# Kernel optimization log

Hardware: AMD Instinct MI355X
Metric: run time of the kernel (lower is better)

Reference implementation:

```python
import jax, jax.numpy as jnp
import numpy as np

N, E = 20000, 320000
H1, C1 = 8, 128   # gat1 heads/out
H2, C2 = 1, 128   # gat2 heads/out
D_IN = 768
NEG_SLOPE = 0.2
BN_EPS = 1e-5


def setup_inputs() -> dict:
    key = jax.random.key(0)
    ks = jax.random.split(key, 16)
    def rn(k, shape, fan):
        return jax.random.normal(k, shape, dtype=jnp.float32) / np.sqrt(fan)
    x = jax.random.normal(ks[0], (N, D_IN), dtype=jnp.float32)
    edge_index = jax.random.randint(ks[1], (2, E), 0, N, dtype=jnp.int64)
    return {
        "x": x,
        "edge_index": edge_index,
        "W1": rn(ks[2], (D_IN, H1 * C1), D_IN),
        "att_src1": rn(ks[3], (H1, C1), C1),
        "att_dst1": rn(ks[4], (H1, C1), C1),
        "b1": jnp.zeros((H1 * C1,), jnp.float32),
        "W2": rn(ks[5], (H1 * C1, H2 * C2), H1 * C1),
        "att_src2": rn(ks[6], (H2, C2), C2),
        "att_dst2": rn(ks[7], (H2, C2), C2),
        "b2": jnp.zeros((C2,), jnp.float32),
        "g1": jnp.ones((H1 * C1,), jnp.float32),
        "be1": jnp.zeros((H1 * C1,), jnp.float32),
        "g2": jnp.ones((C2,), jnp.float32),
        "be2": jnp.zeros((C2,), jnp.float32),
        "Wc1": rn(ks[8], (C2, 64), C2),
        "bc1": jnp.zeros((64,), jnp.float32),
        "Wc2": rn(ks[9], (64, 2), 64),
        "bc2": jnp.zeros((2,), jnp.float32),
    }


def gat_conv(x, src, dst, W, att_src, att_dst, bias, heads, ch, concat):
    n = x.shape[0]
    h = (x @ W).reshape(n, heads, ch)                      # [N,H,C]
    a_s = jnp.sum(h * att_src[None], axis=-1)              # [N,H]
    a_d = jnp.sum(h * att_dst[None], axis=-1)
    e = a_s[src] + a_d[dst]                                # [Et,H]
    e = jax.nn.leaky_relu(e, NEG_SLOPE)
    # segment softmax over incoming edges of each dst node
    m = jax.ops.segment_max(e, dst, num_segments=n)
    ex = jnp.exp(e - m[dst])
    z = jax.ops.segment_sum(ex, dst, num_segments=n)
    alpha = ex / z[dst]                                    # [Et,H]
    msg = alpha[:, :, None] * h[src]                       # [Et,H,C]
    out = jax.ops.segment_sum(msg, dst, num_segments=n)    # [N,H,C]
    if concat:
        out = out.reshape(n, heads * ch)
    else:
        out = out.mean(axis=1)
    return out + bias


def batch_norm(x, gamma, beta):
    mu = x.mean(axis=0)
    var = x.var(axis=0)
    return (x - mu) * jax.lax.rsqrt(var + BN_EPS) * gamma + beta


def reference(x, edge_index, W1, att_src1, att_dst1, b1, W2, att_src2, att_dst2, b2,
              g1, be1, g2, be2, Wc1, bc1, Wc2, bc2):
    n = x.shape[0]
    loop = jnp.arange(n, dtype=edge_index.dtype)
    src = jnp.concatenate([edge_index[0], loop])  # PyG add_self_loops default
    dst = jnp.concatenate([edge_index[1], loop])
    h = gat_conv(x, src, dst, W1, att_src1, att_dst1, b1, H1, C1, True)
    h = jax.nn.elu(batch_norm(h, g1, be1))
    h = gat_conv(h, src, dst, W2, att_src2, att_dst2, b2, H2, C2, False)
    h = jax.nn.elu(batch_norm(h, g2, be2))
    h = jax.nn.relu(h @ Wc1 + bc1)
    return h @ Wc2 + bc2
```

## Files before the change

### kernel.cpp

```cpp
#include <hip/hip_runtime.h>
#include <hip/hip_bf16.h>
#include <math.h>

#define N_NODES 20000
#define N_EDGES 320000
#define DIN 768
#define F1 1024
#define H1 8
#define C1 128
#define F2 128
#define NEG_SLOPE 0.2f
#define BN_EPS 1e-5f
#define RESCALE_THR 8.0f

typedef __attribute__((ext_vector_type(8))) __bf16 bf16x8;
typedef __attribute__((ext_vector_type(4))) float f32x4;

__device__ __forceinline__ float leaky(float x) { return x > 0.f ? x : NEG_SLOPE * x; }

__device__ __forceinline__ unsigned short f2bu(float x) {
  __hip_bfloat16 b = __float2bfloat16(x);
  return *(unsigned short*)&b;
}
__device__ __forceinline__ float b2f(unsigned short u) {
  return __uint_as_float(((unsigned)u) << 16);
}
__device__ __forceinline__ unsigned pack2(float lo, float hi) {
  return (unsigned)f2bu(lo) | ((unsigned)f2bu(hi) << 16);
}

__device__ __forceinline__ void async_copy16(void* lds, const void* g) {
  __builtin_amdgcn_global_load_lds(
      (const __attribute__((address_space(1))) unsigned int*)g,
      (__attribute__((address_space(3))) unsigned int*)lds, 16, 0, 0);
}

__global__ void repack_hist_kernel(const int* raw, int* ei32, int* deg) {
  int is64 = (raw[1] == 0 && raw[3] == 0 && raw[5] == 0 && raw[7] == 0) ? 1 : 0;
  int e = blockIdx.x * blockDim.x + threadIdx.x;
  if (e < 2 * N_EDGES) {
    int v = is64 ? raw[2 * e] : raw[e];
    ei32[e] = v;
    if (e >= N_EDGES) atomicAdd(&deg[v], 1);
  }
}

#define NPT 20
__global__ __launch_bounds__(1024) void scan_kernel(const int* __restrict__ deg,
                                                    int* __restrict__ off,
                                                    int* __restrict__ cursor) {
  __shared__ int wsum[16];
  int tid = threadIdx.x;
  int lane = tid & 63, wv = tid >> 6;
  int base = tid * NPT;
  int loc[NPT];
  int run = 0;
#pragma unroll
  for (int k = 0; k < NPT; ++k) {
    int i = base + k;
    int v = (i < N_NODES) ? deg[i] : 0;
    loc[k] = run;
    run += v;
  }
  int incl = run;
  for (int sh = 1; sh < 64; sh <<= 1) {
    int t = __shfl_up(incl, sh, 64);
    if (lane >= sh) incl += t;
  }
  if (lane == 63) wsum[wv] = incl;
  __syncthreads();
  if (wv == 0 && lane < 16) {
    int v = wsum[lane];
    for (int sh = 1; sh < 16; sh <<= 1) {
      int t = __shfl_up(v, sh, 16);
      if (lane >= sh) v += t;
    }
    wsum[lane] = v;
  }
  __syncthreads();
  int wbase = (wv > 0) ? wsum[wv - 1] : 0;
  int tbase = wbase + incl - run;
#pragma unroll
  for (int k = 0; k < NPT; ++k) {
    int i = base + k;
    if (i < N_NODES) {
      int o = tbase + loc[k];
      off[i] = o;
      cursor[i] = o;
    }
  }
  if (tid == 1023) off[N_NODES] = wbase + incl;
}

__global__ void scatter_kernel(const int* ei, int* cursor, int* elist) {
  int e = blockIdx.x * blockDim.x + threadIdx.x;
  if (e < N_EDGES) {
    int dst = ei[N_EDGES + e];
    int p = atomicAdd(&cursor[dst], 1);
    elist[p] = ei[e];
  }
}

__global__ void f2b_kernel(const float* __restrict__ in, unsigned short* __restrict__ out,
                           size_t n4) {
  size_t i = (size_t)blockIdx.x * blockDim.x + threadIdx.x;
  size_t stride = (size_t)gridDim.x * blockDim.x;
  for (; i < n4; i += stride) {
    float4 v = ((const float4*)in)[i];
    ushort4 u;
    u.x = f2bu(v.x); u.y = f2bu(v.y); u.z = f2bu(v.z); u.w = f2bu(v.w);
    ((ushort4*)out)[i] = u;
  }
}

__global__ void transpose_b_kernel(const float* __restrict__ W, unsigned short* __restrict__ WT,
                                   int K, int N) {
  __shared__ float t[32][33];
  int k0 = blockIdx.y * 32, n0 = blockIdx.x * 32;
  int tx = threadIdx.x & 31, ty = threadIdx.x >> 5;
  for (int i = 0; i < 32; i += 8)
    t[ty + i][tx] = W[(size_t)(k0 + ty + i) * N + n0 + tx];
  __syncthreads();
  for (int i = 0; i < 32; i += 8)
    WT[(size_t)(n0 + ty + i) * K + k0 + tx] = f2bu(t[tx][ty + i]);
}

#define GBM 128
#define GBN 128
#define GBK 64
template <int H, int SWZ>
__global__ __launch_bounds__(256) void mfma_gemm_att_kernel(
    const unsigned short* __restrict__ A,
    const unsigned short* __restrict__ BT,
    unsigned short* __restrict__ C,
    const float* __restrict__ att_src,
    const float* __restrict__ att_dst,
    float* __restrict__ as_out,
    float* __restrict__ ad_out,
    int M, int N, int K) {
  __shared__ __hip_bfloat16 As[GBM][GBK];
  __shared__ __hip_bfloat16 Bs[GBN][GBK];
  __shared__ float sred[128][2];
  __shared__ float dred[128][2];
  int bx, by;
  if (SWZ) {
    int bid = blockIdx.x;
    int pl = bid & 7, c = (bid >> 3) & 7, ph = bid >> 6;
    int p = ph * 8 + pl;
    if (p * GBM >= M) return;
    by = p; bx = c;
  } else {
    bx = blockIdx.x; by = blockIdx.y;
  }
  int tid = threadIdx.x;
  int lane = tid & 63, wid = tid >> 6;
  int wr = wid >> 1, wc = wid & 1;
  int row0 = by * GBM, col0 = bx * GBN;
  int head = bx;
  int l16 = lane & 15, l4 = lane >> 4;
  f32x4 acc[4][4] = {};
  for (int k0 = 0; k0 < K; k0 += GBK) {
#pragma unroll
    for (int j = 0; j < 4; ++j) {
      int c = j * 256 + tid;
      int r = c >> 3, kk = (c & 7) << 3;
      int ga = row0 + r; if (ga >= M) ga = M - 1;
      async_copy16(&As[r][kk], A + (size_t)ga * K + k0 + kk);
      async_copy16(&Bs[r][kk], BT + (size_t)(col0 + r) * K + k0 + kk);
    }
    __syncthreads();
#pragma unroll
    for (int ks = 0; ks < 2; ++ks) {
      bf16x8 af[4], bfr[4];
#pragma unroll
      for (int i = 0; i < 4; ++i)
        af[i] = *(const bf16x8*)&As[wr * 64 + i * 16 + l16][ks * 32 + l4 * 8];
#pragma unroll
      for (int j = 0; j < 4; ++j)
        bfr[j] = *(const bf16x8*)&Bs[wc * 64 + j * 16 + l16][ks * 32 + l4 * 8];
#pragma unroll
      for (int i = 0; i < 4; ++i)
#pragma unroll
        for (int j = 0; j < 4; ++j)
          acc[i][j] = __builtin_amdgcn_mfma_f32_16x16x32_bf16(af[i], bfr[j], acc[i][j], 0, 0, 0);
    }
    __syncthreads();
  }
#pragma unroll
  for (int i = 0; i < 4; ++i) {
#pragma unroll
    for (int j = 0; j < 4; ++j) {
#pragma unroll
      for (int r = 0; r < 4; ++r) {
        int row = row0 + wr * 64 + i * 16 + l4 * 4 + r;
        int col = col0 + wc * 64 + j * 16 + l16;
        if (row < M) C[(size_t)row * N + col] = f2bu(acc[i][j][r]);
      }
    }
  }
  float avs[4], avd[4];
#pragma unroll
  for (int j = 0; j < 4; ++j) {
    int col = col0 + wc * 64 + j * 16 + l16;
    avs[j] = att_src[col];
    avd[j] = att_dst[col];
  }
#pragma unroll
  for (int i = 0; i < 4; ++i) {
#pragma unroll
    for (int r = 0; r < 4; ++r) {
      float ps = 0.f, pd = 0.f;
#pragma unroll
      for (int j = 0; j < 4; ++j) { ps += acc[i][j][r] * avs[j]; pd += acc[i][j][r] * avd[j]; }
#pragma unroll
      for (int mk = 1; mk < 16; mk <<= 1) {
        ps += __shfl_xor(ps, mk, 64);
        pd += __shfl_xor(pd, mk, 64);
      }
      if (l16 == 0) {
        int lr = wr * 64 + i * 16 + l4 * 4 + r;
        sred[lr][wc] = ps;
        dred[lr][wc] = pd;
      }
    }
  }
  __syncthreads();
  if (tid < 128) {
    int row = row0 + tid;
    if (row < M) {
      as_out[(size_t)row * H + head] = sred[tid][0] + sred[tid][1];
      ad_out[(size_t)row * H + head] = dred[tid][0] + dred[tid][1];
    }
  }
}

#define G1_LOAD(i, rv, ev)                                                     \
  if ((i) < e) {                                                               \
    int ssrc = elist[(i)];                                                     \
    ev = leaky(as1[ssrc * H1 + head] + ad);                                    \
    rv = *(const uint4*)(h1 + (size_t)ssrc * F1 + tid * 8);                    \
  }
#define G1_CONSUME(u, el)                                                      \
  {                                                                            \
    float w;                                                                   \
    if (el > m + RESCALE_THR) {                                                \
      float rr = __expf(m - el);                                               \
      z *= rr;                                                                 \
      acc0 *= rr; acc1 *= rr; acc2 *= rr; acc3 *= rr;                          \
      acc4 *= rr; acc5 *= rr; acc6 *= rr; acc7 *= rr;                          \
      m = el; w = 1.f;                                                         \
    } else {                                                                   \
      w = __expf(el - m);                                                      \
    }                                                                          \
    z += w;                                                                    \
    acc0 += w * __uint_as_float(u.x << 16);                                    \
    acc1 += w * __uint_as_float(u.x & 0xffff0000u);                            \
    acc2 += w * __uint_as_float(u.y << 16);                                    \
    acc3 += w * __uint_as_float(u.y & 0xffff0000u);                            \
    acc4 += w * __uint_as_float(u.z << 16);                                    \
    acc5 += w * __uint_as_float(u.z & 0xffff0000u);                            \
    acc6 += w * __uint_as_float(u.w << 16);                                    \
    acc7 += w * __uint_as_float(u.w & 0xffff0000u);                            \
  }

__global__ __launch_bounds__(128) void gather1_kernel(const unsigned short* __restrict__ h1,
                                                      const float* __restrict__ as1,
                                                      const float* __restrict__ ad1,
                                                      const int* __restrict__ off,
                                                      const int* __restrict__ elist,
                                                      const float* __restrict__ b1,
                                                      unsigned short* __restrict__ out1) {
  int node = blockIdx.x;
  int tid = threadIdx.x;
  int head = tid >> 4;
  const float ad = ad1[node * H1 + head];
  int s = off[node], e = off[node + 1];
  float m = leaky(as1[node * H1 + head] + ad);
  float z = 1.f;
  float acc0, acc1, acc2, acc3, acc4, acc5, acc6, acc7;
  {
    uint4 u = *(const uint4*)(h1 + (size_t)node * F1 + tid * 8);
    acc0 = __uint_as_float(u.x << 16); acc1 = __uint_as_float(u.x & 0xffff0000u);
    acc2 = __uint_as_float(u.y << 16); acc3 = __uint_as_float(u.y & 0xffff0000u);
    acc4 = __uint_as_float(u.z << 16); acc5 = __uint_as_float(u.z & 0xffff0000u);
    acc6 = __uint_as_float(u.w << 16); acc7 = __uint_as_float(u.w & 0xffff0000u);
  }
  uint4 ra0 = {}, ra1 = {}, ra2 = {}, ra3 = {};
  float ea0 = 0.f, ea1 = 0.f, ea2 = 0.f, ea3 = 0.f;
  G1_LOAD(s + 0, ra0, ea0)
  G1_LOAD(s + 1, ra1, ea1)
  G1_LOAD(s + 2, ra2, ea2)
  G1_LOAD(s + 3, ra3, ea3)
  for (int base = s; base < e; base += 4) {
    uint4 rb0 = {}, rb1 = {}, rb2 = {}, rb3 = {};
    float eb0 = 0.f, eb1 = 0.f, eb2 = 0.f, eb3 = 0.f;
    int nb = base + 4;
    G1_LOAD(nb + 0, rb0, eb0)
    G1_LOAD(nb + 1, rb1, eb1)
    G1_LOAD(nb + 2, rb2, eb2)
    G1_LOAD(nb + 3, rb3, eb3)
    G1_CONSUME(ra0, ea0)
    if (base + 1 < e) G1_CONSUME(ra1, ea1)
    if (base + 2 < e) G1_CONSUME(ra2, ea2)
    if (base + 3 < e) G1_CONSUME(ra3, ea3)
    ra0 = rb0; ra1 = rb1; ra2 = rb2; ra3 = rb3;
    ea0 = eb0; ea1 = eb1; ea2 = eb2; ea3 = eb3;
  }
  float inv = 1.f / z;
  const float4 bv0 = *(const float4*)(b1 + tid * 8);
  const float4 bv1 = *(const float4*)(b1 + tid * 8 + 4);
  uint4 o;
  o.x = pack2(acc0 * inv + bv0.x, acc1 * inv + bv0.y);
  o.y = pack2(acc2 * inv + bv0.z, acc3 * inv + bv0.w);
  o.z = pack2(acc4 * inv + bv1.x, acc5 * inv + bv1.y);
  o.w = pack2(acc6 * inv + bv1.z, acc7 * inv + bv1.w);
  *(uint4*)(out1 + (size_t)node * F1 + tid * 8) = o;
}

__global__ void bnstats_bf16_kernel(const unsigned short* __restrict__ x,
                                    float* __restrict__ sums,
                                    int nrows, int F, int rowsPerBlock) {
  int tid = threadIdx.x;
  int c = tid * 4;
  int r0 = blockIdx.x * rowsPerBlock;
  int rend = min(r0 + rowsPerBlock, nrows);
  float s0 = 0.f, s1 = 0.f, s2 = 0.f, s3 = 0.f;
  float q0 = 0.f, q1 = 0.f, q2 = 0.f, q3 = 0.f;
  for (int r = r0; r < rend; ++r) {
    ushort4 u = *(const ushort4*)(x + (size_t)r * F + c);
    float v0 = b2f(u.x), v1 = b2f(u.y), v2 = b2f(u.z), v3 = b2f(u.w);
    s0 += v0; s1 += v1; s2 += v2; s3 += v3;
    q0 += v0 * v0; q1 += v1 * v1; q2 += v2 * v2; q3 += v3 * v3;
  }
  atomicAdd(&sums[c + 0], s0); atomicAdd(&sums[c + 1], s1);
  atomicAdd(&sums[c + 2], s2); atomicAdd(&sums[c + 3], s3);
  atomicAdd(&sums[F + c + 0], q0); atomicAdd(&sums[F + c + 1], q1);
  atomicAdd(&sums[F + c + 2], q2); atomicAdd(&sums[F + c + 3], q3);
}

template <int CPT>
__global__ void bnstats_kernel(const float* __restrict__ x, float* __restrict__ sums,
                               int nrows, int F, int rowsPerBlock) {
  int tid = threadIdx.x;
  int r0 = blockIdx.x * rowsPerBlock;
  int rend = min(r0 + rowsPerBlock, nrows);
  float s[CPT], q[CPT];
#pragma unroll
  for (int k = 0; k < CPT; ++k) { s[k] = 0.f; q[k] = 0.f; }
  for (int r = r0; r < rend; ++r) {
    const float* row = x + (size_t)r * F;
#pragma unroll
    for (int k = 0; k < CPT; ++k) {
      float v = row[tid + k * blockDim.x];
      s[k] += v; q[k] += v * v;
    }
  }
#pragma unroll
  for (int k = 0; k < CPT; ++k) {
    atomicAdd(&sums[tid + k * blockDim.x], s[k]);
    atomicAdd(&sums[F + tid + k * blockDim.x], q[k]);
  }
}

__global__ void bnfinal_kernel(const float* __restrict__ sums, const float* __restrict__ g,
                               const float* __restrict__ be, float* __restrict__ ss, int F) {
  int c = blockIdx.x * blockDim.x + threadIdx.x;
  if (c < F) {
    float mu = sums[c] * (1.f / N_NODES);
    float var = sums[F + c] * (1.f / N_NODES) - mu * mu;
    float sc = g[c] * rsqrtf(var + BN_EPS);
    ss[c] = sc;
    ss[F + c] = be[c] - mu * sc;
  }
}

__global__ void bnapply_bf16_kernel(unsigned short* __restrict__ x, const float* __restrict__ ss,
                                    int F, size_t total4) {
  size_t i = (size_t)blockIdx.x * blockDim.x + threadIdx.x;
  size_t stride = (size_t)gridDim.x * blockDim.x;
  for (; i < total4; i += stride) {
    int c = (int)((i * 4) & (size_t)(F - 1));
    ushort4 u = ((ushort4*)x)[i];
    float v0 = b2f(u.x) * ss[c + 0] + ss[F + c + 0];
    float v1 = b2f(u.y) * ss[c + 1] + ss[F + c + 1];
    float v2 = b2f(u.z) * ss[c + 2] + ss[F + c + 2];
    float v3 = b2f(u.w) * ss[c + 3] + ss[F + c + 3];
    v0 = v0 > 0.f ? v0 : expm1f(v0);
    v1 = v1 > 0.f ? v1 : expm1f(v1);
    v2 = v2 > 0.f ? v2 : expm1f(v2);
    v3 = v3 > 0.f ? v3 : expm1f(v3);
    u.x = f2bu(v0); u.y = f2bu(v1); u.z = f2bu(v2); u.w = f2bu(v3);
    ((ushort4*)x)[i] = u;
  }
}

#define G2_LOAD(i, rv, ev)                                                     \
  if ((i) < e) {                                                               \
    int ssrc = elist[(i)];                                                     \
    ev = leaky(as2[ssrc] + ad);                                                \
    rv = *(const unsigned*)(h2 + (size_t)ssrc * F2 + tid * 2);                 \
  }
#define G2_CONSUME(u, el)                                                      \
  {                                                                            \
    float w;                                                                   \
    if (el > m + RESCALE_THR) {                                                \
      float rr = __expf(m - el);                                               \
      z *= rr; a0 *= rr; a1 *= rr;                                             \
      m = el; w = 1.f;                                                         \
    } else {                                                                   \
      w = __expf(el - m);                                                      \
    }                                                                          \
    z += w;                                                                    \
    a0 += w * __uint_as_float(u << 16);                                        \
    a1 += w * __uint_as_float(u & 0xffff0000u);                                \
  }

__global__ __launch_bounds__(64) void gather2_kernel(const unsigned short* __restrict__ h2,
                                                     const float* __restrict__ as2,
                                                     const float* __restrict__ ad2,
                                                     const int* __restrict__ off,
                                                     const int* __restrict__ elist,
                                                     const float* __restrict__ b2,
                                                     float* __restrict__ out2) {
  int node = blockIdx.x;
  int tid = threadIdx.x;
  const float ad = ad2[node];
  int s = off[node], e = off[node + 1];
  float m = leaky(as2[node] + ad);
  float z = 1.f;
  float a0, a1;
  {
    unsigned u = *(const unsigned*)(h2 + (size_t)node * F2 + tid * 2);
    a0 = __uint_as_float(u << 16); a1 = __uint_as_float(u & 0xffff0000u);
  }
  unsigned ra0 = 0, ra1 = 0, ra2 = 0, ra3 = 0;
  float ea0 = 0.f, ea1 = 0.f, ea2 = 0.f, ea3 = 0.f;
  G2_LOAD(s + 0, ra0, ea0)
  G2_LOAD(s + 1, ra1, ea1)
  G2_LOAD(s + 2, ra2, ea2)
  G2_LOAD(s + 3, ra3, ea3)
  for (int base = s; base < e; base += 4) {
    unsigned rb0 = 0, rb1 = 0, rb2 = 0, rb3 = 0;
    float eb0 = 0.f, eb1 = 0.f, eb2 = 0.f, eb3 = 0.f;
    int nb = base + 4;
    G2_LOAD(nb + 0, rb0, eb0)
    G2_LOAD(nb + 1, rb1, eb1)
    G2_LOAD(nb + 2, rb2, eb2)
    G2_LOAD(nb + 3, rb3, eb3)
    G2_CONSUME(ra0, ea0)
    if (base + 1 < e) G2_CONSUME(ra1, ea1)
    if (base + 2 < e) G2_CONSUME(ra2, ea2)
    if (base + 3 < e) G2_CONSUME(ra3, ea3)
    ra0 = rb0; ra1 = rb1; ra2 = rb2; ra3 = rb3;
    ea0 = eb0; ea1 = eb1; ea2 = eb2; ea3 = eb3;
  }
  float inv = 1.f / z;
  float2 o = make_float2(a0 * inv + b2[tid * 2 + 0], a1 * inv + b2[tid * 2 + 1]);
  *(float2*)(out2 + (size_t)node * F2 + tid * 2) = o;
}

__global__ __launch_bounds__(64) void cls_kernel(const float* __restrict__ h,
                                                 const float* __restrict__ ss2,
                                                 const float* __restrict__ Wc1,
                                                 const float* __restrict__ bc1,
                                                 const float* __restrict__ Wc2,
                                                 const float* __restrict__ bc2,
                                                 float* __restrict__ out) {
  __shared__ float hl[128];
  int node = blockIdx.x;
  int tid = threadIdx.x;
  {
    float v = h[(size_t)node * F2 + tid] * ss2[tid] + ss2[F2 + tid];
    v = v > 0.f ? v : expm1f(v);
    hl[tid] = v;
    float v2 = h[(size_t)node * F2 + 64 + tid] * ss2[64 + tid] + ss2[F2 + 64 + tid];
    v2 = v2 > 0.f ? v2 : expm1f(v2);
    hl[tid + 64] = v2;
  }
  __syncthreads();
  float acc = bc1[tid];
#pragma unroll
  for (int k = 0; k < 128; ++k) acc += hl[k] * Wc1[k * 64 + tid];
  acc = fmaxf(acc, 0.f);
  float2 w = *(const float2*)(Wc2 + tid * 2);
  float o0 = acc * w.x, o1 = acc * w.y;
  for (int sh = 32; sh >= 1; sh >>= 1) {
    o0 += __shfl_down(o0, sh, 64);
    o1 += __shfl_down(o1, sh, 64);
  }
  if (tid == 0) {
    out[node * 2 + 0] = o0 + bc2[0];
    out[node * 2 + 1] = o1 + bc2[1];
  }
}

extern "C" void kernel_launch(void* const* d_in, const int* in_sizes, int n_in,
                              void* d_out, int out_size, void* d_ws, size_t ws_size,
                              hipStream_t stream) {
  const float* x        = (const float*)d_in[0];
  const int*   ei_raw   = (const int*)d_in[1];
  const float* W1       = (const float*)d_in[2];
  const float* att_src1 = (const float*)d_in[3];
  const float* att_dst1 = (const float*)d_in[4];
  const float* b1       = (const float*)d_in[5];
  const float* W2       = (const float*)d_in[6];
  const float* att_src2 = (const float*)d_in[7];
  const float* att_dst2 = (const float*)d_in[8];
  const float* b2       = (const float*)d_in[9];
  const float* g1       = (const float*)d_in[10];
  const float* be1      = (const float*)d_in[11];
  const float* g2       = (const float*)d_in[12];
  const float* be2      = (const float*)d_in[13];
  const float* Wc1      = (const float*)d_in[14];
  const float* bc1      = (const float*)d_in[15];
  const float* Wc2      = (const float*)d_in[16];
  const float* bc2      = (const float*)d_in[17];
  float* out = (float*)d_out;

  char* ws = (char*)d_ws;
  size_t o = 0;
  unsigned short* h1b   = (unsigned short*)(ws + o); o += (size_t)N_NODES * F1 * 2;
  unsigned short* out1b = (unsigned short*)(ws + o); o += (size_t)N_NODES * F1 * 2;
  unsigned short* xb    = (unsigned short*)(ws + o); o += (size_t)N_NODES * DIN * 2;
  unsigned short* h2b   = (unsigned short*)(ws + o); o += (size_t)N_NODES * F2 * 2;
  float* out2  = (float*)(ws + o); o += (size_t)N_NODES * F2 * 4;
  float* as1   = (float*)(ws + o); o += (size_t)N_NODES * H1 * 4;
  float* ad1   = (float*)(ws + o); o += (size_t)N_NODES * H1 * 4;
  float* as2   = (float*)(ws + o); o += (size_t)N_NODES * 4;
  float* ad2   = (float*)(ws + o); o += (size_t)N_NODES * 4;
  char*  zbase = ws + o;
  float* bnsum1 = (float*)(ws + o); o += F1 * 2 * 4;
  float* bnsum2 = (float*)(ws + o); o += F2 * 2 * 4;
  int*   deg    = (int*)(ws + o); o += (size_t)N_NODES * 4;
  size_t zbytes = (size_t)((ws + o) - zbase);
  int*   offv   = (int*)(ws + o); o += (size_t)(N_NODES + 4) * 4;
  int*   cursor = (int*)(ws + o); o += (size_t)N_NODES * 4;
  int*   elist  = (int*)(ws + o); o += (size_t)N_EDGES * 4;
  float* ss1    = (float*)(ws + o); o += F1 * 2 * 4;
  float* ss2    = (float*)(ws + o); o += F2 * 2 * 4;
  int*   ei32   = (int*)(ws + o); o += (size_t)2 * N_EDGES * 4;
  unsigned short* W1T = (unsigned short*)(ws + o); o += (size_t)F1 * DIN * 2;
  unsigned short* W2T = (unsigned short*)(ws + o); o += (size_t)F2 * F1 * 2;
  (void)ws_size; (void)in_sizes; (void)n_in; (void)out_size;

  hipMemsetAsync((void*)zbase, 0, zbytes, stream);

  f2b_kernel<<<2048, 256, 0, stream>>>(x, xb, (size_t)N_NODES * DIN / 4);
  {
    dim3 g1d(F1 / 32, DIN / 32);
    transpose_b_kernel<<<g1d, 256, 0, stream>>>(W1, W1T, DIN, F1);
    dim3 g2d(F2 / 32, F1 / 32);
    transpose_b_kernel<<<g2d, 256, 0, stream>>>(W2, W2T, F1, F2);
  }

  repack_hist_kernel<<<(2 * N_EDGES + 255) / 256, 256, 0, stream>>>(ei_raw, ei32, deg);
  scan_kernel<<<1, 1024, 0, stream>>>(deg, offv, cursor);
  scatter_kernel<<<(N_EDGES + 255) / 256, 256, 0, stream>>>(ei32, cursor, elist);

  {
    int panels = (N_NODES + GBM - 1) / GBM;
    int grid1 = ((panels + 7) / 8) * 64;
    mfma_gemm_att_kernel<H1, 1><<<grid1, 256, 0, stream>>>(
        xb, W1T, h1b, att_src1, att_dst1, as1, ad1, N_NODES, F1, DIN);
  }
  gather1_kernel<<<N_NODES, 128, 0, stream>>>(h1b, as1, ad1, offv, elist, b1, out1b);
  {
    int rows = 79;
    int grid = (N_NODES + rows - 1) / rows;
    bnstats_bf16_kernel<<<grid, 256, 0, stream>>>(out1b, bnsum1, N_NODES, F1, rows);
  }
  bnfinal_kernel<<<(F1 + 255) / 256, 256, 0, stream>>>(bnsum1, g1, be1, ss1, F1);
  bnapply_bf16_kernel<<<2048, 256, 0, stream>>>(out1b, ss1, F1, (size_t)N_NODES * F1 / 4);

  {
    dim3 grid(F2 / GBN, (N_NODES + GBM - 1) / GBM);
    mfma_gemm_att_kernel<1, 0><<<grid, 256, 0, stream>>>(
        out1b, W2T, h2b, att_src2, att_dst2, as2, ad2, N_NODES, F2, F1);
  }
  gather2_kernel<<<N_NODES, 64, 0, stream>>>(h2b, as2, ad2, offv, elist, b2, out2);
  {
    int rows = 79;
    int grid = (N_NODES + rows - 1) / rows;
    bnstats_kernel<1><<<grid, 128, 0, stream>>>(out2, bnsum2, N_NODES, F2, rows);
  }
  bnfinal_kernel<<<1, F2, 0, stream>>>(bnsum2, g2, be2, ss2, F2);

  cls_kernel<<<N_NODES, 64, 0, stream>>>(out2, ss2, Wc1, bc1, Wc2, bc2, out);
}
```

Baseline: 427.2 us.

## Split GAT layer-1 gather into one 64-thread block per node-head pair

The layer-1 gather is remapped from one 128-thread block per node (each thread handling 8 channels with 16-byte loads) to a 2D grid of 64-thread blocks, one per (head, node), where each thread handles 2 channels with 4-byte loads. This gives eight times more blocks and far fewer live registers per thread, aiming for more memory-level parallelism and better latency hiding on the random row gathers. In exchange, each block redoes the edge-list and attention-score loads per head, and the narrower per-thread loads may lower memory efficiency per instruction.

```diff
diff --git a/kernel.cpp b/kernel.cpp
--- a/kernel.cpp
+++ b/kernel.cpp
@@ -238,61 +238,51 @@
   if ((i) < e) {                                                               \
     int ssrc = elist[(i)];                                                     \
     ev = leaky(as1[ssrc * H1 + head] + ad);                                    \
-    rv = *(const uint4*)(h1 + (size_t)ssrc * F1 + tid * 8);                    \
+    rv = *(const unsigned*)(h1 + (size_t)ssrc * F1 + cb);                      \
   }
 #define G1_CONSUME(u, el)                                                      \
   {                                                                            \
     float w;                                                                   \
     if (el > m + RESCALE_THR) {                                                \
       float rr = __expf(m - el);                                               \
-      z *= rr;                                                                 \
-      acc0 *= rr; acc1 *= rr; acc2 *= rr; acc3 *= rr;                          \
-      acc4 *= rr; acc5 *= rr; acc6 *= rr; acc7 *= rr;                          \
+      z *= rr; a0 *= rr; a1 *= rr;                                             \
       m = el; w = 1.f;                                                         \
     } else {                                                                   \
       w = __expf(el - m);                                                      \
     }                                                                          \
     z += w;                                                                    \
-    acc0 += w * __uint_as_float(u.x << 16);                                    \
-    acc1 += w * __uint_as_float(u.x & 0xffff0000u);                            \
-    acc2 += w * __uint_as_float(u.y << 16);                                    \
-    acc3 += w * __uint_as_float(u.y & 0xffff0000u);                            \
-    acc4 += w * __uint_as_float(u.z << 16);                                    \
-    acc5 += w * __uint_as_float(u.z & 0xffff0000u);                            \
-    acc6 += w * __uint_as_float(u.w << 16);                                    \
-    acc7 += w * __uint_as_float(u.w & 0xffff0000u);                            \
-  }
-
-__global__ __launch_bounds__(128) void gather1_kernel(const unsigned short* __restrict__ h1,
-                                                      const float* __restrict__ as1,
-                                                      const float* __restrict__ ad1,
-                                                      const int* __restrict__ off,
-                                                      const int* __restrict__ elist,
-                                                      const float* __restrict__ b1,
-                                                      unsigned short* __restrict__ out1) {
-  int node = blockIdx.x;
-  int tid = threadIdx.x;
-  int head = tid >> 4;
+    a0 += w * __uint_as_float(u << 16);                                        \
+    a1 += w * __uint_as_float(u & 0xffff0000u);                                \
+  }
+
+__global__ __launch_bounds__(64) void gather1_kernel(const unsigned short* __restrict__ h1,
+                                                     const float* __restrict__ as1,
+                                                     const float* __restrict__ ad1,
+                                                     const int* __restrict__ off,
+                                                     const int* __restrict__ elist,
+                                                     const float* __restrict__ b1,
+                                                     unsigned short* __restrict__ out1) {
+  int head = blockIdx.x;
+  int node = blockIdx.y;
+  int tid = threadIdx.x;
+  int cb = head * C1 + tid * 2;
   const float ad = ad1[node * H1 + head];
   int s = off[node], e = off[node + 1];
   float m = leaky(as1[node * H1 + head] + ad);
   float z = 1.f;
-  float acc0, acc1, acc2, acc3, acc4, acc5, acc6, acc7;
-  {
-    uint4 u = *(const uint4*)(h1 + (size_t)node * F1 + tid * 8);
-    acc0 = __uint_as_float(u.x << 16); acc1 = __uint_as_float(u.x & 0xffff0000u);
-    acc2 = __uint_as_float(u.y << 16); acc3 = __uint_as_float(u.y & 0xffff0000u);
-    acc4 = __uint_as_float(u.z << 16); acc5 = __uint_as_float(u.z & 0xffff0000u);
-    acc6 = __uint_as_float(u.w << 16); acc7 = __uint_as_float(u.w & 0xffff0000u);
-  }
-  uint4 ra0 = {}, ra1 = {}, ra2 = {}, ra3 = {};
+  float a0, a1;
+  {
+    unsigned u = *(const unsigned*)(h1 + (size_t)node * F1 + cb);
+    a0 = __uint_as_float(u << 16); a1 = __uint_as_float(u & 0xffff0000u);
+  }
+  unsigned ra0 = 0, ra1 = 0, ra2 = 0, ra3 = 0;
   float ea0 = 0.f, ea1 = 0.f, ea2 = 0.f, ea3 = 0.f;
   G1_LOAD(s + 0, ra0, ea0)
   G1_LOAD(s + 1, ra1, ea1)
   G1_LOAD(s + 2, ra2, ea2)
   G1_LOAD(s + 3, ra3, ea3)
   for (int base = s; base < e; base += 4) {
-    uint4 rb0 = {}, rb1 = {}, rb2 = {}, rb3 = {};
+    unsigned rb0 = 0, rb1 = 0, rb2 = 0, rb3 = 0;
     float eb0 = 0.f, eb1 = 0.f, eb2 = 0.f, eb3 = 0.f;
     int nb = base + 4;
     G1_LOAD(nb + 0, rb0, eb0)
@@ -307,14 +297,9 @@
     ea0 = eb0; ea1 = eb1; ea2 = eb2; ea3 = eb3;
   }
   float inv = 1.f / z;
-  const float4 bv0 = *(const float4*)(b1 + tid * 8);
-  const float4 bv1 = *(const float4*)(b1 + tid * 8 + 4);
-  uint4 o;
-  o.x = pack2(acc0 * inv + bv0.x, acc1 * inv + bv0.y);
-  o.y = pack2(acc2 * inv + bv0.z, acc3 * inv + bv0.w);
-  o.z = pack2(acc4 * inv + bv1.x, acc5 * inv + bv1.y);
-  o.w = pack2(acc6 * inv + bv1.z, acc7 * inv + bv1.w);
-  *(uint4*)(out1 + (size_t)node * F1 + tid * 8) = o;
+  float2 bv = *(const float2*)(b1 + cb);
+  unsigned o = pack2(a0 * inv + bv.x, a1 * inv + bv.y);
+  *(unsigned*)(out1 + (size_t)node * F1 + cb) = o;
 }
 
 __global__ void bnstats_bf16_kernel(const unsigned short* __restrict__ x,
@@ -563,7 +548,7 @@
     mfma_gemm_att_kernel<H1, 1><<<grid1, 256, 0, stream>>>(
         xb, W1T, h1b, att_src1, att_dst1, as1, ad1, N_NODES, F1, DIN);
   }
-  gather1_kernel<<<N_NODES, 128, 0, stream>>>(h1b, as1, ad1, offv, elist, b1, out1b);
+  gather1_kernel<<<dim3(H1, N_NODES), 64, 0, stream>>>(h1b, as1, ad1, offv, elist, b1, out1b);
   {
     int rows = 79;
     int grid = (N_NODES + rows - 1) / rows;
```

New measurement: 477.1 us. +11.7%, slower.
